# Kernel optimization log

Hardware: AMD Instinct MI355X
Metric: run time of the kernel (lower is better)

## Reference

```python
import jax, jax.numpy as jnp
import numpy as np
import math

B, LQ, LK, D = 8, 128, 256, 32
ET, H, NH = 32, 8, 64
ETK = ET // H  # 4
LN_EPS = 1e-5


def setup_inputs() -> dict:
    key = jax.random.key(0)
    ks = jax.random.split(key, 12)
    s = 0.02
    return {
        "query_tt": jax.random.uniform(ks[0], (B, LQ), jnp.float32),
        "key_tt": jax.random.uniform(ks[1], (B, LK), jnp.float32),
        "value": jax.random.normal(ks[2], (B, LK, D), jnp.float32),
        "emb_mask": jax.random.randint(ks[3], (B, LK, D), 0, 2, jnp.int32),
        "w_time": jax.random.normal(ks[4], (1, 1), jnp.float32) * s,
        "b_time": jnp.zeros((1,), jnp.float32),
        "w_periodic": jax.random.normal(ks[5], (ET - 1,), jnp.float32) * s,
        "b_periodic": jnp.zeros((ET - 1,), jnp.float32),
        "w_decay": jnp.array([[0.1]], jnp.float32),
        "vt_w1": jax.random.normal(ks[6], (D, NH), jnp.float32) * s,
        "vt_b1": jnp.zeros((NH,), jnp.float32),
        "ln_g": jnp.ones((NH,), jnp.float32),
        "ln_b": jnp.zeros((NH,), jnp.float32),
        "vt_w2": jax.random.normal(ks[7], (NH, D), jnp.float32) * s,
        "vt_b2": jnp.zeros((D,), jnp.float32),
        "wq": jax.random.normal(ks[8], (ET, ET), jnp.float32) * s,
        "bq": jnp.zeros((ET,), jnp.float32),
        "wk": jax.random.normal(ks[9], (ET, ET), jnp.float32) * s,
        "bk": jnp.zeros((ET,), jnp.float32),
        "wo": jax.random.normal(ks[10], (H * D, NH), jnp.float32) * s,
        "bo": jnp.zeros((NH,), jnp.float32),
    }


def _forward(query_tt, key_tt, value, emb_mask, w_time, b_time, w_periodic, b_periodic,
             w_decay, vt_w1, vt_b1, ln_g, ln_b, vt_w2, vt_b2, wq, bq, wk, bk, wo, bo):
    Bv, Lq = query_tt.shape
    Lk = key_tt.shape[1]
    Dv = value.shape[-1]

    # ---- value transfer embedding ----
    v = jnp.broadcast_to(value[:, None, :, :], (Bv, Lq, Lk, Dv))  # [B,Lq,Lk,D]
    d_t = query_tt[:, :, None] - key_tt[:, None, :]               # [B,Lq,Lk]
    hdn = v @ vt_w1 + vt_b1                                       # [B,Lq,Lk,NH]
    mu = hdn.mean(-1, keepdims=True)
    var = ((hdn - mu) ** 2).mean(-1, keepdims=True)
    hdn = (hdn - mu) * jax.lax.rsqrt(var + LN_EPS) * ln_g + ln_b  # LayerNorm
    hdn = jax.nn.relu(hdn)
    d_value = hdn @ vt_w2 + vt_b2                                 # [B,Lq,Lk,D]
    dt1 = d_t[..., None]                                          # [B,Lq,Lk,1]
    time_decay = 1.0 / (1.0 + dt1 * w_decay[0, 0])
    v = d_value * time_decay * dt1 + v                            # [B,Lq,Lk,D]

    # ---- learned time embedding ----
    def time_emb(tt):
        t = tt[..., None]  # [B,L,1]
        return jnp.concatenate([t * w_time[0, 0] + b_time,
                                jnp.sin(t * w_periodic + b_periodic)], axis=-1)  # [B,L,ET]

    q = (time_emb(query_tt) @ wq + bq).reshape(Bv, Lq, H, ETK).transpose(0, 2, 1, 3)  # [B,h,Lq,etk]
    k = (time_emb(key_tt) @ wk + bk).reshape(Bv, Lk, H, ETK).transpose(0, 2, 1, 3)    # [B,h,Lk,etk]

    # ---- per-value-dim attention ----
    scores = jnp.einsum('bhqe,bhke->bhqk', q, k) / math.sqrt(ETK)          # [B,h,Lq,Lk]
    mask5 = emb_mask[:, None, None, :, :]                                   # [B,1,1,Lk,D]
    scores5 = jnp.where(mask5 == 0, jnp.float32(-10000.0), scores[..., None])  # [B,h,Lq,Lk,D]
    p_attn = jax.nn.softmax(scores5, axis=-2)                               # softmax over Lk, per dim d
    x = jnp.einsum('bhqkd,bqkd->bhqd', p_attn, v)                           # [B,h,Lq,D]
    x = x.transpose(0, 2, 1, 3).reshape(Bv, Lq, H * Dv)
    return x @ wo + bo                                                      # [B,Lq,NH]


def reference(query_tt, key_tt, value, emb_mask, w_time, b_time, w_periodic, b_periodic,
              w_decay, vt_w1, vt_b1, ln_g, ln_b, vt_w2, vt_b2, wq, bq, wk, bk, wo, bo):
    return _forward(query_tt, key_tt, value, emb_mask, w_time, b_time, w_periodic, b_periodic,
                    w_decay, vt_w1, vt_b1, ln_g, ln_b, vt_w2, vt_b2, wq, bq, wk, bk, wo, bo)
```

## Files before the change

kernel.cpp:

```cpp
#include <hip/hip_runtime.h>

#define Bv_ 8
#define LQ 128
#define LK 256
#define Dv 32
#define ET 32
#define Hh 8
#define NH 64

__global__ __launch_bounds__(64) void prep_kernel(
    const float* __restrict__ qtt, const float* __restrict__ ktt,
    const float* __restrict__ value, const int* __restrict__ emb_mask,
    const float* __restrict__ w_time, const float* __restrict__ b_time,
    const float* __restrict__ w_per, const float* __restrict__ b_per,
    const float* __restrict__ vt_w1, const float* __restrict__ vt_b1,
    const float* __restrict__ ln_g, const float* __restrict__ ln_b,
    const float* __restrict__ vt_w2, const float* __restrict__ vt_b2,
    const float* __restrict__ wq, const float* __restrict__ bq,
    const float* __restrict__ wk, const float* __restrict__ bk,
    float* __restrict__ A, float* __restrict__ Bdv, float* __restrict__ mf,
    float* __restrict__ qe, float* __restrict__ ke)
{
    const int t = threadIdx.x;
    const int blk = blockIdx.x;

    if (blk < Bv_ * LK) {
        __shared__ float vrow[Dv];
        __shared__ float hrow[NH];
        const int row = blk;
        if (t < Dv) vrow[t] = value[row * Dv + t];
        __syncthreads();

        float h = vt_b1[t];
        #pragma unroll
        for (int d = 0; d < Dv; ++d) h += vrow[d] * vt_w1[d * NH + t];

        float s = h;
        #pragma unroll
        for (int off = 32; off > 0; off >>= 1) s += __shfl_xor(s, off);
        const float mu = s * (1.0f / NH);
        const float dc = h - mu;
        float vs = dc * dc;
        #pragma unroll
        for (int off = 32; off > 0; off >>= 1) vs += __shfl_xor(vs, off);
        const float var = vs * (1.0f / NH);
        const float rs = rsqrtf(var + 1e-5f);
        float hn = dc * rs * ln_g[t] + ln_b[t];
        hn = fmaxf(hn, 0.0f);
        hrow[t] = hn;
        __syncthreads();

        if (t < Dv) {
            float dval = vt_b2[t];
            #pragma unroll
            for (int j = 0; j < NH; ++j) dval += hrow[j] * vt_w2[j * Dv + t];
            const int m = emb_mask[row * Dv + t];
            const float mm = (m != 0) ? 1.0f : 0.0f;
            A[row * Dv + t]   = mm * vrow[t];
            Bdv[row * Dv + t] = mm * dval;
            mf[row * Dv + t]  = mm;
        }
    } else {
        const int idx = blk - Bv_ * LK;
        const int sub = t >> 5;
        const int j = t & 31;
        const int row = idx * 2 + sub;
        __shared__ float eb[2][ET];

        float tt;
        const float *W, *bias;
        float* outp;
        if (row < Bv_ * LQ) {
            tt = qtt[row];
            W = wq; bias = bq; outp = qe + row * ET;
        } else {
            const int r2 = row - Bv_ * LQ;
            tt = ktt[r2];
            W = wk; bias = bk; outp = ke + r2 * ET;
        }
        float e;
        if (j == 0) e = tt * w_time[0] + b_time[0];
        else        e = sinf(tt * w_per[j - 1] + b_per[j - 1]);
        eb[sub][j] = e;
        __syncthreads();

        float o = bias[j];
        #pragma unroll
        for (int i = 0; i < ET; ++i) o += eb[sub][i] * W[i * ET + j];
        outp[j] = o;
    }
}

__global__ __launch_bounds__(256) void attn_kernel(
    const float* __restrict__ qtt, const float* __restrict__ ktt,
    const float* __restrict__ w_decay,
    const float* __restrict__ A, const float* __restrict__ Bdv,
    const float* __restrict__ mf,
    const float* __restrict__ qe, const float* __restrict__ ke,
    const float* __restrict__ wo, const float* __restrict__ bo,
    float* __restrict__ out)
{
    __shared__ float Eh[Hh][LK];
    __shared__ float gk[LK];
    __shared__ float qrow[ET];
    __shared__ float xsh[Hh * Dv];
    __shared__ float psum[4][NH];

    const int t = threadIdx.x;
    const int bq_ = blockIdx.x;
    const int b = bq_ >> 7;

    if (t < ET) qrow[t] = qe[bq_ * ET + t];
    {
        const float dt = qtt[bq_] - ktt[b * LK + t];
        gk[t] = dt / (1.0f + w_decay[0] * dt);
    }
    __syncthreads();
    {
        const float4* kerow = (const float4*)(ke + (b * LK + t) * ET);
        #pragma unroll
        for (int h = 0; h < Hh; ++h) {
            const float4 kk = kerow[h];
            const float sc = 0.5f * (qrow[4*h]   * kk.x + qrow[4*h+1] * kk.y +
                                     qrow[4*h+2] * kk.z + qrow[4*h+3] * kk.w);
            Eh[h][t] = expf(sc);
        }
    }
    __syncthreads();

    {
        const int h = t >> 5, d = t & 31;
        const float* Ab = A   + b * LK * Dv + d;
        const float* Bb = Bdv + b * LK * Dv + d;
        const float* Mb = mf  + b * LK * Dv + d;
        float num = 0.0f, den = 0.0f;
        #pragma unroll 8
        for (int k = 0; k < LK; ++k) {
            const float e = Eh[h][k];
            const float a = Ab[k * Dv];
            const float bb = Bb[k * Dv];
            const float m = Mb[k * Dv];
            num += e * (a + gk[k] * bb);
            den += e * m;
        }
        xsh[t] = num / fmaxf(den, 1e-30f);
    }
    __syncthreads();

    {
        const int j = t & 63, quarter = t >> 6;
        float p = 0.0f;
        #pragma unroll
        for (int c0 = 0; c0 < 64; ++c0) {
            const int c = quarter * 64 + c0;
            p += xsh[c] * wo[c * NH + j];
        }
        psum[quarter][j] = p;
    }
    __syncthreads();
    if (t < NH) {
        out[bq_ * NH + t] = bo[t] + psum[0][t] + psum[1][t] + psum[2][t] + psum[3][t];
    }
}

extern "C" void kernel_launch(void* const* d_in, const int* in_sizes, int n_in,
                              void* d_out, int out_size, void* d_ws, size_t ws_size,
                              hipStream_t stream) {
    const float* qtt      = (const float*)d_in[0];
    const float* ktt      = (const float*)d_in[1];
    const float* value    = (const float*)d_in[2];
    const int*   emb_mask = (const int*)  d_in[3];
    const float* w_time   = (const float*)d_in[4];
    const float* b_time   = (const float*)d_in[5];
    const float* w_per    = (const float*)d_in[6];
    const float* b_per    = (const float*)d_in[7];
    const float* w_decay  = (const float*)d_in[8];
    const float* vt_w1    = (const float*)d_in[9];
    const float* vt_b1    = (const float*)d_in[10];
    const float* ln_g     = (const float*)d_in[11];
    const float* ln_b     = (const float*)d_in[12];
    const float* vt_w2    = (const float*)d_in[13];
    const float* vt_b2    = (const float*)d_in[14];
    const float* wq       = (const float*)d_in[15];
    const float* bq       = (const float*)d_in[16];
    const float* wk       = (const float*)d_in[17];
    const float* bk       = (const float*)d_in[18];
    const float* wo       = (const float*)d_in[19];
    const float* bo       = (const float*)d_in[20];
    float* out = (float*)d_out;

    float* ws  = (float*)d_ws;
    float* Aw  = ws;
    float* Bw  = ws + 65536;
    float* Mw  = ws + 131072;
    float* qew = ws + 196608;
    float* kew = ws + 229376;

    const int nblk_prep = Bv_ * LK + (Bv_ * LQ + Bv_ * LK) / 2;
    hipLaunchKernelGGL(prep_kernel, dim3(nblk_prep), dim3(64), 0, stream,
                       qtt, ktt, value, emb_mask, w_time, b_time, w_per, b_per,
                       vt_w1, vt_b1, ln_g, ln_b, vt_w2, vt_b2,
                       wq, bq, wk, bk, Aw, Bw, Mw, qew, kew);

    hipLaunchKernelGGL(attn_kernel, dim3(Bv_ * LQ), dim3(256), 0, stream,
                       qtt, ktt, w_decay, Aw, Bw, Mw, qew, kew, wo, bo, out);
}
```

Measured before the change: 127.9 us.

## Vectorize attention accumulation with float4 and split key range across wave groups

The attention reduction now has each thread accumulate four value dimensions through float4 loads over a quarter of the keys. Partial numerators and denominators are combined in shared memory, which replaces the scalar strided loads over all 256 keys per thread. The prep kernel packs four value rows (or eight time-embedding rows) per 256-thread block, which cuts the block count. Fast __expf/__sinf intrinsics replace the precise versions. This adds an extra reduction pass and sync and slightly lowers transcendental accuracy.

```diff
diff --git a/kernel.cpp b/kernel.cpp
--- a/kernel.cpp
+++ b/kernel.cpp
@@ -8,7 +8,7 @@
 #define Hh 8
 #define NH 64
 
-__global__ __launch_bounds__(64) void prep_kernel(
+__global__ __launch_bounds__(256) void prep_kernel(
     const float* __restrict__ qtt, const float* __restrict__ ktt,
     const float* __restrict__ value, const int* __restrict__ emb_mask,
     const float* __restrict__ w_time, const float* __restrict__ b_time,
@@ -24,16 +24,19 @@
     const int t = threadIdx.x;
     const int blk = blockIdx.x;
 
-    if (blk < Bv_ * LK) {
-        __shared__ float vrow[Dv];
-        __shared__ float hrow[NH];
-        const int row = blk;
-        if (t < Dv) vrow[t] = value[row * Dv + t];
+    if (blk < 512) {
+        __shared__ float vrow[4][Dv];
+        __shared__ float hrow[4][NH];
+        const int w = t >> 6;
+        const int l = t & 63;
+        const int row = blk * 4 + w;
+
+        if (l < Dv) vrow[w][l] = value[row * Dv + l];
         __syncthreads();
 
-        float h = vt_b1[t];
-        #pragma unroll
-        for (int d = 0; d < Dv; ++d) h += vrow[d] * vt_w1[d * NH + t];
+        float h = vt_b1[l];
+        #pragma unroll
+        for (int d = 0; d < Dv; ++d) h += vrow[w][d] * vt_w1[d * NH + l];
 
         float s = h;
         #pragma unroll
@@ -43,29 +46,26 @@
         float vs = dc * dc;
         #pragma unroll
         for (int off = 32; off > 0; off >>= 1) vs += __shfl_xor(vs, off);
-        const float var = vs * (1.0f / NH);
-        const float rs = rsqrtf(var + 1e-5f);
-        float hn = dc * rs * ln_g[t] + ln_b[t];
-        hn = fmaxf(hn, 0.0f);
-        hrow[t] = hn;
+        const float rs = rsqrtf(vs * (1.0f / NH) + 1e-5f);
+        float hn = dc * rs * ln_g[l] + ln_b[l];
+        hrow[w][l] = fmaxf(hn, 0.0f);
         __syncthreads();
 
-        if (t < Dv) {
-            float dval = vt_b2[t];
+        if (l < Dv) {
+            float dval = vt_b2[l];
             #pragma unroll
-            for (int j = 0; j < NH; ++j) dval += hrow[j] * vt_w2[j * Dv + t];
-            const int m = emb_mask[row * Dv + t];
-            const float mm = (m != 0) ? 1.0f : 0.0f;
-            A[row * Dv + t]   = mm * vrow[t];
-            Bdv[row * Dv + t] = mm * dval;
-            mf[row * Dv + t]  = mm;
+            for (int j = 0; j < NH; ++j) dval += hrow[w][j] * vt_w2[j * Dv + l];
+            const float mm = (emb_mask[row * Dv + l] != 0) ? 1.0f : 0.0f;
+            A[row * Dv + l]   = mm * vrow[w][l];
+            Bdv[row * Dv + l] = mm * dval;
+            mf[row * Dv + l]  = mm;
         }
     } else {
-        const int idx = blk - Bv_ * LK;
+        const int idx = blk - 512;
         const int sub = t >> 5;
         const int j = t & 31;
-        const int row = idx * 2 + sub;
-        __shared__ float eb[2][ET];
+        const int row = idx * 8 + sub;
+        __shared__ float eb[8][ET];
 
         float tt;
         const float *W, *bias;
@@ -80,7 +80,7 @@
         }
         float e;
         if (j == 0) e = tt * w_time[0] + b_time[0];
-        else        e = sinf(tt * w_per[j - 1] + b_per[j - 1]);
+        else        e = __sinf(tt * w_per[j - 1] + b_per[j - 1]);
         eb[sub][j] = e;
         __syncthreads();
 
@@ -100,60 +100,90 @@
     const float* __restrict__ wo, const float* __restrict__ bo,
     float* __restrict__ out)
 {
-    __shared__ float Eh[Hh][LK];
+    __shared__ float Eh[Hh][LK + 4];
     __shared__ float gk[LK];
-    __shared__ float qrow[ET];
-    __shared__ float xsh[Hh * Dv];
+    __shared__ float4 qrow4[Hh];
+    __shared__ float4 psN[4][64];
+    __shared__ float4 psD[4][64];
+    __shared__ float4 xsh4[64];
     __shared__ float psum[4][NH];
 
     const int t = threadIdx.x;
     const int bq_ = blockIdx.x;
     const int b = bq_ >> 7;
 
-    if (t < ET) qrow[t] = qe[bq_ * ET + t];
+    if (t < ET) ((float*)qrow4)[t] = qe[bq_ * ET + t];
     {
         const float dt = qtt[bq_] - ktt[b * LK + t];
-        gk[t] = dt / (1.0f + w_decay[0] * dt);
-    }
-    __syncthreads();
+        gk[t] = dt / fmaf(w_decay[0], dt, 1.0f);
+    }
+    __syncthreads();
+
     {
         const float4* kerow = (const float4*)(ke + (b * LK + t) * ET);
         #pragma unroll
         for (int h = 0; h < Hh; ++h) {
             const float4 kk = kerow[h];
-            const float sc = 0.5f * (qrow[4*h]   * kk.x + qrow[4*h+1] * kk.y +
-                                     qrow[4*h+2] * kk.z + qrow[4*h+3] * kk.w);
-            Eh[h][t] = expf(sc);
-        }
-    }
-    __syncthreads();
-
-    {
-        const int h = t >> 5, d = t & 31;
-        const float* Ab = A   + b * LK * Dv + d;
-        const float* Bb = Bdv + b * LK * Dv + d;
-        const float* Mb = mf  + b * LK * Dv + d;
-        float num = 0.0f, den = 0.0f;
-        #pragma unroll 8
-        for (int k = 0; k < LK; ++k) {
-            const float e = Eh[h][k];
-            const float a = Ab[k * Dv];
-            const float bb = Bb[k * Dv];
-            const float m = Mb[k * Dv];
-            num += e * (a + gk[k] * bb);
-            den += e * m;
-        }
-        xsh[t] = num / fmaxf(den, 1e-30f);
+            const float4 qq = qrow4[h];
+            const float sc = 0.5f * (qq.x * kk.x + qq.y * kk.y +
+                                     qq.z * kk.z + qq.w * kk.w);
+            Eh[h][t] = __expf(sc);
+        }
+    }
+    __syncthreads();
+
+    {
+        const int ks = t >> 6;
+        const int h  = (t >> 3) & 7;
+        const int d4 = t & 7;
+        const float4* Ab = (const float4*)(A   + (size_t)b * LK * Dv) + d4;
+        const float4* Bb = (const float4*)(Bdv + (size_t)b * LK * Dv) + d4;
+        const float4* Mb = (const float4*)(mf  + (size_t)b * LK * Dv) + d4;
+        float4 num = {0.f, 0.f, 0.f, 0.f};
+        float4 den = {0.f, 0.f, 0.f, 0.f};
+        const int k0 = ks * 64;
+        #pragma unroll 4
+        for (int kk = 0; kk < 64; ++kk) {
+            const int k = k0 + kk;
+            const float e  = Eh[h][k];
+            const float eg = e * gk[k];
+            const float4 a = Ab[k * 8];
+            const float4 bb = Bb[k * 8];
+            const float4 m = Mb[k * 8];
+            num.x += e * a.x + eg * bb.x;
+            num.y += e * a.y + eg * bb.y;
+            num.z += e * a.z + eg * bb.z;
+            num.w += e * a.w + eg * bb.w;
+            den.x += e * m.x;
+            den.y += e * m.y;
+            den.z += e * m.z;
+            den.w += e * m.w;
+        }
+        psN[ks][t & 63] = num;
+        psD[ks][t & 63] = den;
+    }
+    __syncthreads();
+
+    if (t < 64) {
+        float4 N0 = psN[0][t], N1 = psN[1][t], N2 = psN[2][t], N3 = psN[3][t];
+        float4 D0 = psD[0][t], D1 = psD[1][t], D2 = psD[2][t], D3 = psD[3][t];
+        float4 x;
+        x.x = (N0.x + N1.x + N2.x + N3.x) / fmaxf(D0.x + D1.x + D2.x + D3.x, 1e-30f);
+        x.y = (N0.y + N1.y + N2.y + N3.y) / fmaxf(D0.y + D1.y + D2.y + D3.y, 1e-30f);
+        x.z = (N0.z + N1.z + N2.z + N3.z) / fmaxf(D0.z + D1.z + D2.z + D3.z, 1e-30f);
+        x.w = (N0.w + N1.w + N2.w + N3.w) / fmaxf(D0.w + D1.w + D2.w + D3.w, 1e-30f);
+        xsh4[t] = x;
     }
     __syncthreads();
 
     {
         const int j = t & 63, quarter = t >> 6;
+        const float* xs = (const float*)xsh4;
         float p = 0.0f;
         #pragma unroll
         for (int c0 = 0; c0 < 64; ++c0) {
             const int c = quarter * 64 + c0;
-            p += xsh[c] * wo[c * NH + j];
+            p += xs[c] * wo[c * NH + j];
         }
         psum[quarter][j] = p;
     }
@@ -196,8 +226,7 @@
     float* qew = ws + 196608;
     float* kew = ws + 229376;
 
-    const int nblk_prep = Bv_ * LK + (Bv_ * LQ + Bv_ * LK) / 2;
-    hipLaunchKernelGGL(prep_kernel, dim3(nblk_prep), dim3(64), 0, stream,
+    hipLaunchKernelGGL(prep_kernel, dim3(896), dim3(256), 0, stream,
                        qtt, ktt, value, emb_mask, w_time, b_time, w_per, b_per,
                        vt_w1, vt_b1, ln_g, ln_b, vt_w2, vt_b2,
                        wq, bq, wk, bk, Aw, Bw, Mw, qew, kew);
```

Measured after the change: 144.8 us. 1.13x slower.
